# Performance work log

Hardware: AMD Instinct MI355X
Metric: run time of the kernel (lower is better)

Reference implementation:

```python
import jax, jax.numpy as jnp
import numpy as np
from jax import lax

NUM_MASKS = 100
NUM_CLASSES = 81  # 80 + 1
KERNEL_DIM = 256
BIAS_PRIOR = float(-np.log((1 - 0.01) / 0.01))


def setup_inputs() -> dict:
    key = jax.random.key(0)
    ks = jax.random.split(key, 12)
    B, C, H, W = 4, 256, 160, 160
    D = C  # expand_dim = in_channels * num_groups
    inp = {
        "features": jax.random.normal(ks[0], (B, C, H, W), jnp.float32),
        # iam_conv: Conv2d(C, num_masks, 3, padding=1)
        "w_iam": jax.random.normal(ks[1], (NUM_MASKS, C, 3, 3), jnp.float32) * 0.01,
        "b_iam": jnp.full((NUM_MASKS,), BIAS_PRIOR, jnp.float32),
        "softmax_bias": jnp.ones((1,), jnp.float32),
        # fc: Linear(D, D), xavier-ish
        "w_fc": jax.random.normal(ks[2], (D, D), jnp.float32) * (1.0 / np.sqrt(D)),
        "b_fc": jnp.zeros((D,), jnp.float32),
        "w_cls": jax.random.normal(ks[3], (NUM_CLASSES, D), jnp.float32) * 0.01,
        "b_cls": jnp.full((NUM_CLASSES,), BIAS_PRIOR, jnp.float32),
        "w_ker": jax.random.normal(ks[4], (KERNEL_DIM, D), jnp.float32) * 0.01,
        "b_ker": jnp.zeros((KERNEL_DIM,), jnp.float32),
        "w_obj": jax.random.normal(ks[5], (1, D), jnp.float32) * (1.0 / np.sqrt(D)),
        "b_obj": jnp.zeros((1,), jnp.float32),
        "w_box": jax.random.normal(ks[6], (4, D), jnp.float32) * 0.01,
        "b_box": jnp.zeros((4,), jnp.float32),
    }
    return inp


def reference(features, w_iam, b_iam, softmax_bias, w_fc, b_fc,
              w_cls, b_cls, w_ker, b_ker, w_obj, b_obj, w_box, b_box):
    B, C, H, W = features.shape
    # conv score map: (B, num_masks, H, W)
    iam = lax.conv_general_dilated(
        features, w_iam, window_strides=(1, 1), padding="SAME",
        dimension_numbers=("NCHW", "OIHW", "NCHW")) + b_iam[None, :, None, None]
    # num_groups == 1: single group iam
    iam_flat = iam.reshape(B, NUM_MASKS, H * W)
    # softmax over HW with learned scalar bias (bias shifts uniformly -> no-op math-wise but kept faithful)
    iam_prob = jax.nn.softmax(iam_flat + softmax_bias[0], axis=-1)  # (B, M, HW)
    # spatial attention pooling: bmm(prob, feats^T) -> (B, M, C)
    inst = jnp.einsum("bmp,bcp->bmc", iam_prob, features.reshape(B, C, H * W))
    # prev_inst_features is None -> skip fc_fuse
    inst = jax.nn.relu(inst @ w_fc.T + b_fc)
    pred_logits = inst @ w_cls.T + b_cls
    pred_kernel = inst @ w_ker.T + b_ker
    pred_scores = inst @ w_obj.T + b_obj
    pred_bboxes = inst @ w_box.T + b_box
    return (pred_logits, pred_kernel, pred_scores, pred_bboxes, iam, inst)
```

## Files before the change

### kernel.cpp

```cpp
#include <hip/hip_runtime.h>
#include <hip/hip_bf16.h>

typedef __attribute__((ext_vector_type(8))) short bf16x8;
typedef __attribute__((ext_vector_type(4))) float f32x4;

#define HW_ 25600
#define HP_ 162
#define WP_ 162

__device__ __forceinline__ unsigned short f2bf(float f) {
    union { float f; unsigned u; } x; x.f = f;
    unsigned r = x.u + 0x7FFFu + ((x.u >> 16) & 1u);
    return (unsigned short)(r >> 16);
}

typedef const __attribute__((address_space(1))) unsigned int* gas_t;
typedef __attribute__((address_space(3))) unsigned int* las_t;
__device__ __forceinline__ void gl_lds16(const void* g, void* l) {
    __builtin_amdgcn_global_load_lds((gas_t)g, (las_t)l, 16, 0, 0);
}

__global__ __launch_bounds__(256) void k_prep(const float* __restrict__ w_iam,
                                              unsigned short* __restrict__ wp,
                                              unsigned short* __restrict__ fpad) {
    int bid = blockIdx.x;
    if (bid < 1152) {
        int idx = bid * 256 + threadIdx.x;
        int stage = idx >> 12;
        int r = idx & 4095;
        int m = r >> 5, cl = r & 31;
        int tap = stage >> 3, kc = stage & 7;
        int jj = (cl >> 3) ^ ((m >> 1) & 3);
        int c = kc * 32 + jj * 8 + (cl & 7);
        int dy = (tap * 11) >> 5, dx = tap - dy * 3;
        float v = (m < 100) ? w_iam[((m * 256 + c) * 3 + dy) * 3 + dx] : 0.f;
        wp[idx] = f2bf(v);
    } else {
        int idx = (bid - 1152) * 256 + threadIdx.x;
        const int perb = 164864;
        if (idx >= 4 * perb) return;
        int b = idx / perb;
        int r = idx - b * perb;
        int hp, wpp, c;
        if (r < 82944) {
            hp = (r < 41472) ? 0 : 161;
            int r2 = r % 41472;
            wpp = r2 >> 8; c = r2 & 255;
        } else {
            r -= 82944;
            wpp = (r < 40960) ? 0 : 161;
            int r2 = r % 40960;
            hp = 1 + (r2 >> 8); c = r2 & 255;
        }
        fpad[((b * HP_ + hp) * WP_ + wpp) * 256 + c] = 0;
    }
}

__global__ __launch_bounds__(256) void k_convert(const float* __restrict__ feat,
                                                 unsigned short* __restrict__ fpad) {
    int bid = blockIdx.x;
    int b = bid / 640;
    int h = (bid >> 2) % 160;
    int c0 = (bid & 3) * 64;
    __shared__ float tile[64][161];
    int t = threadIdx.x;
    const float4* src4 = (const float4*)(feat + ((long)(b * 256 + c0) * 160 + h) * 160);
    #pragma unroll
    for (int s = 0; s < 10; ++s) {
        int q = t + s * 256;
        int ci = q / 40;
        int w4 = q - ci * 40;
        float4 v = src4[(long)ci * 6400 + w4];
        tile[ci][w4 * 4 + 0] = v.x;
        tile[ci][w4 * 4 + 1] = v.y;
        tile[ci][w4 * 4 + 2] = v.z;
        tile[ci][w4 * 4 + 3] = v.w;
    }
    __syncthreads();
    int co = (t & 7) * 8, wq = t >> 3;
    unsigned short* dst = fpad + ((long)(b * HP_ + h + 1) * WP_ + 1) * 256 + c0 + co;
    #pragma unroll
    for (int wp = 0; wp < 5; ++wp) {
        int w = wq + wp * 32;
        bf16x8 v;
        #pragma unroll
        for (int j = 0; j < 8; ++j) v[j] = (short)f2bf(tile[co + j][w]);
        *(bf16x8*)(dst + (long)w * 256) = v;
    }
}

__global__ __launch_bounds__(256, 3) void k_conv(const unsigned short* __restrict__ fpad,
                                                 const unsigned short* __restrict__ wprep,
                                                 const float* __restrict__ b_iam,
                                                 float* __restrict__ iam) {
    int bid = blockIdx.x;
    bid = (bid & 7) * 100 + (bid >> 3);
    int b = bid / 200;
    int p0 = (bid % 200) * 128;
    int tid = threadIdx.x;
    int lane = tid & 63, wid = tid >> 6;
    int wr = wid >> 1, wc = wid & 1;

    __shared__ __align__(16) unsigned short As[2][4096];
    __shared__ __align__(16) unsigned short Bs[2][4096];

    const unsigned short* fb = fpad + (long)b * HP_ * WP_ * 256;
    const unsigned short* gBsrc[2];
    {
        int swz = ((lane & 3) ^ ((lane >> 3) & 3)) * 8;
        #pragma unroll
        for (int i = 0; i < 2; ++i) {
            int pr = i * 64 + wid * 16 + (lane >> 2);
            int p = p0 + pr;
            int h = p / 160, w = p - h * 160;
            gBsrc[i] = fb + ((long)h * WP_ + w) * 256 + swz;
        }
    }
    const unsigned short* gA0 = wprep + (wid << 9) + (lane << 3);

    f32x4 acc[4][4];
    #pragma unroll
    for (int i = 0; i < 4; ++i)
        #pragma unroll
        for (int j = 0; j < 4; ++j)
            #pragma unroll
            for (int k = 0; k < 4; ++k) acc[i][j][k] = 0.f;

    int chB   = (((lane >> 4) ^ ((lane >> 1) & 3)) << 4);
    int aBase = (wr << 12) + ((lane & 15) << 6) + chB;
    int bBase = (wc << 12) + ((lane & 15) << 6) + chB;

    auto issue = [&](int s, int bi) {
        int tap = s >> 3, kc = s & 7;
        int dy = (tap * 11) >> 5, dx = tap - dy * 3;
        long boff = ((long)dy * WP_ + dx) * 256 + kc * 32;
        const unsigned short* ga = gA0 + ((long)s << 12);
        char* Ad = (char*)As[bi] + (wid << 10);
        char* Bd = (char*)Bs[bi] + (wid << 10);
        gl_lds16(ga, Ad);
        gl_lds16(ga + 2048, Ad + 4096);
        gl_lds16(gBsrc[0] + boff, Bd);
        gl_lds16(gBsrc[1] + boff, Bd + 4096);
    };

    auto compute = [&](int bi) {
        const char* Ab = (const char*)As[bi];
        const char* Bb = (const char*)Bs[bi];
        bf16x8 af[4], bfv[4];
        #pragma unroll
        for (int mf = 0; mf < 4; ++mf)
            af[mf] = *(const bf16x8*)(Ab + aBase + (mf << 10));
        #pragma unroll
        for (int nf = 0; nf < 4; ++nf)
            bfv[nf] = *(const bf16x8*)(Bb + bBase + (nf << 10));
        __builtin_amdgcn_s_setprio(1);
        #pragma unroll
        for (int mf = 0; mf < 4; ++mf)
            #pragma unroll
            for (int nf = 0; nf < 4; ++nf)
                acc[mf][nf] = __builtin_amdgcn_mfma_f32_16x16x32_bf16(
                    af[mf], bfv[nf], acc[mf][nf], 0, 0, 0);
        __builtin_amdgcn_s_setprio(0);
    };

    issue(0, 0);
    for (int s = 0; s < 71; ++s) {
        issue(s + 1, (s + 1) & 1);
        asm volatile("s_waitcnt vmcnt(4)" ::: "memory");
        __builtin_amdgcn_sched_barrier(0);
        __builtin_amdgcn_s_barrier();
        __builtin_amdgcn_sched_barrier(0);
        compute(s & 1);
        __builtin_amdgcn_sched_barrier(0);
        __builtin_amdgcn_s_barrier();
        __builtin_amdgcn_sched_barrier(0);
    }
    asm volatile("s_waitcnt vmcnt(0)" ::: "memory");
    __builtin_amdgcn_sched_barrier(0);
    __builtin_amdgcn_s_barrier();
    __builtin_amdgcn_sched_barrier(0);
    compute(1);

    float* dst = iam + (long)b * 100 * HW_;
    #pragma unroll
    for (int mf = 0; mf < 4; ++mf)
        #pragma unroll
        for (int nf = 0; nf < 4; ++nf) {
            int p = p0 + wc * 64 + nf * 16 + (lane & 15);
            int m0 = wr * 64 + mf * 16 + ((lane >> 4) << 2);
            #pragma unroll
            for (int j = 0; j < 4; ++j) {
                int m = m0 + j;
                if (m < 100) dst[(long)m * HW_ + p] = acc[mf][nf][j] + b_iam[m];
            }
        }
}

__global__ __launch_bounds__(256, 2) void k_pool(const float* __restrict__ feat,
                                                 const float* __restrict__ iam,
                                                 float* __restrict__ partials,
                                                 float* __restrict__ psum) {
    int bid = blockIdx.x;
    int b = bid / 100;
    int slice = bid - b * 100;
    int p0 = slice * 256;
    int tid = threadIdx.x, lane = tid & 63, wq = tid >> 6;

    __shared__ __align__(16) unsigned short A[128 * 72];
    __shared__ __align__(16) unsigned short Bl[256 * 72];
    __shared__ float sums[128];
    if (tid < 128) sums[tid] = 0.f;
    __syncthreads();

    f32x4 acc[7][4];
    #pragma unroll
    for (int i = 0; i < 7; ++i)
        #pragma unroll
        for (int j = 0; j < 4; ++j)
            #pragma unroll
            for (int k = 0; k < 4; ++k) acc[i][j][k] = 0.f;

    int kgrp = (lane >> 4) << 3;

    for (int ks = 0; ks < 4; ++ks) {
        int k0 = p0 + ks * 64;
        for (int s = 0; s < 4; ++s) {
            int q = tid + s * 256;
            int mi = q >> 3, j0 = (q & 7) * 8;
            bf16x8 o;
            if (mi < 100) {
                const float4* sp4 = (const float4*)(iam + (long)(b * 100 + mi) * HW_ + k0 + j0);
                float4 v0 = sp4[0], v1 = sp4[1];
                float xv[8] = {v0.x, v0.y, v0.z, v0.w, v1.x, v1.y, v1.z, v1.w};
                float ls = 0.f;
                #pragma unroll
                for (int j = 0; j < 8; ++j) {
                    float e = __expf(xv[j]);
                    o[j] = (short)f2bf(e);
                    ls += e;
                }
                atomicAdd(&sums[mi], ls);
            } else {
                #pragma unroll
                for (int j = 0; j < 8; ++j) o[j] = 0;
            }
            *(bf16x8*)(A + mi * 72 + j0) = o;
        }
        for (int s = 0; s < 8; ++s) {
            int q = tid + s * 256;
            int ci = q >> 3, j0 = (q & 7) * 8;
            const float4* sp4 = (const float4*)(feat + (long)(b * 256 + ci) * HW_ + k0 + j0);
            float4 v0 = sp4[0], v1 = sp4[1];
            float xv[8] = {v0.x, v0.y, v0.z, v0.w, v1.x, v1.y, v1.z, v1.w};
            bf16x8 o;
            #pragma unroll
            for (int j = 0; j < 8; ++j) o[j] = (short)f2bf(xv[j]);
            *(bf16x8*)(Bl + ci * 72 + j0) = o;
        }
        __syncthreads();
        #pragma unroll
        for (int kk = 0; kk < 64; kk += 32) {
            bf16x8 af[7], bfv[4];
            #pragma unroll
            for (int mf = 0; mf < 7; ++mf)
                af[mf] = *(const bf16x8*)(A + (mf * 16 + (lane & 15)) * 72 + kk + kgrp);
            #pragma unroll
            for (int nf = 0; nf < 4; ++nf)
                bfv[nf] = *(const bf16x8*)(Bl + (wq * 64 + nf * 16 + (lane & 15)) * 72 + kk + kgrp);
            #pragma unroll
            for (int mf = 0; mf < 7; ++mf)
                #pragma unroll
                for (int nf = 0; nf < 4; ++nf)
                    acc[mf][nf] = __builtin_amdgcn_mfma_f32_16x16x32_bf16(
                        af[mf], bfv[nf], acc[mf][nf], 0, 0, 0);
        }
        __syncthreads();
    }
    if (tid < 100) psum[(long)bid * 112 + tid] = sums[tid];
    float* dst = partials + (long)bid * 112 * 256;
    #pragma unroll
    for (int mf = 0; mf < 7; ++mf)
        #pragma unroll
        for (int nf = 0; nf < 4; ++nf) {
            int m0 = mf * 16 + ((lane >> 4) << 2);
            int c  = wq * 64 + nf * 16 + (lane & 15);
            #pragma unroll
            for (int j = 0; j < 4; ++j)
                dst[(long)(m0 + j) * 256 + c] = acc[mf][nf][j];
        }
}

__global__ __launch_bounds__(256) void k_redpool(const float* __restrict__ partials,
                                                 const float* __restrict__ psum,
                                                 float* __restrict__ inst_pool) {
    int bid = blockIdx.x;
    int b = bid / 100, m = bid - b * 100;
    int c = threadIdx.x;
    float s = 0.f, d = 0.f;
    for (int sl = 0; sl < 100; ++sl) {
        s += partials[((long)(b * 100 + sl) * 112 + m) * 256 + c];
        d += psum[(long)(b * 100 + sl) * 112 + m];
    }
    inst_pool[(long)bid * 256 + c] = s / d;
}

__global__ __launch_bounds__(256) void k_fc(const float* __restrict__ inst_pool,
                                            const float* __restrict__ w_fc, const float* __restrict__ b_fc,
                                            const float* __restrict__ w_cls, const float* __restrict__ b_cls,
                                            const float* __restrict__ w_ker, const float* __restrict__ b_ker,
                                            const float* __restrict__ w_obj, const float* __restrict__ b_obj,
                                            const float* __restrict__ w_box, const float* __restrict__ b_box,
                                            float* __restrict__ out) {
    int r = blockIdx.x;
    int t = threadIdx.x;
    __shared__ float row[256];
    __shared__ float inst_s[256];
    row[t] = inst_pool[(long)r * 256 + t];
    __syncthreads();
    {
        float acc = b_fc[t];
        const float4* wv = (const float4*)(w_fc + (long)t * 256);
        for (int c = 0; c < 64; ++c) {
            float4 w4 = wv[c];
            acc += w4.x * row[c * 4] + w4.y * row[c * 4 + 1] + w4.z * row[c * 4 + 2] + w4.w * row[c * 4 + 3];
        }
        acc = fmaxf(acc, 0.f);
        inst_s[t] = acc;
        out[10376800 + (long)r * 256 + t] = acc;
    }
    __syncthreads();
    {
        float acc = b_ker[t];
        const float4* wv = (const float4*)(w_ker + (long)t * 256);
        for (int c = 0; c < 64; ++c) {
            float4 w4 = wv[c];
            acc += w4.x * inst_s[c * 4] + w4.y * inst_s[c * 4 + 1] + w4.z * inst_s[c * 4 + 2] + w4.w * inst_s[c * 4 + 3];
        }
        out[32400 + (long)r * 256 + t] = acc;
    }
    if (t < 81) {
        float acc = b_cls[t];
        const float4* wv = (const float4*)(w_cls + (long)t * 256);
        for (int c = 0; c < 64; ++c) {
            float4 w4 = wv[c];
            acc += w4.x * inst_s[c * 4] + w4.y * inst_s[c * 4 + 1] + w4.z * inst_s[c * 4 + 2] + w4.w * inst_s[c * 4 + 3];
        }
        out[(long)r * 81 + t] = acc;
    }
    if (t == 0) {
        float acc = b_obj[0];
        for (int c = 0; c < 256; ++c) acc += w_obj[c] * inst_s[c];
        out[134800 + r] = acc;
    }
    if (t >= 1 && t < 5) {
        int j = t - 1;
        float acc = b_box[j];
        for (int c = 0; c < 256; ++c) acc += w_box[j * 256 + c] * inst_s[c];
        out[135200 + (long)r * 4 + j] = acc;
    }
}

extern "C" void kernel_launch(void* const* d_in, const int* in_sizes, int n_in,
                              void* d_out, int out_size, void* d_ws, size_t ws_size,
                              hipStream_t stream) {
    const float* feat  = (const float*)d_in[0];
    const float* w_iam = (const float*)d_in[1];
    const float* b_iam = (const float*)d_in[2];
    const float* w_fc  = (const float*)d_in[4];
    const float* b_fc  = (const float*)d_in[5];
    const float* w_cls = (const float*)d_in[6];
    const float* b_cls = (const float*)d_in[7];
    const float* w_ker = (const float*)d_in[8];
    const float* b_ker = (const float*)d_in[9];
    const float* w_obj = (const float*)d_in[10];
    const float* b_obj = (const float*)d_in[11];
    const float* w_box = (const float*)d_in[12];
    const float* b_box = (const float*)d_in[13];
    float* out = (float*)d_out;

    char* ws = (char*)d_ws;
    unsigned short* fpad  = (unsigned short*)ws;
    unsigned short* wprep = (unsigned short*)(ws + 53747712);
    float* partials  = (float*)ws;
    float* psum      = (float*)(ws + 45875200);
    float* inst_pool = (float*)(ws + 46054400);

    float* iam = out + 136800;

    k_prep   <<<dim3(3728), dim3(256), 0, stream>>>(w_iam, wprep, fpad);
    k_convert<<<dim3(2560), dim3(256), 0, stream>>>(feat, fpad);
    k_conv   <<<dim3(800),  dim3(256), 0, stream>>>(fpad, wprep, b_iam, iam);
    k_pool   <<<dim3(400),  dim3(256), 0, stream>>>(feat, iam, partials, psum);
    k_redpool<<<dim3(400),  dim3(256), 0, stream>>>(partials, psum, inst_pool);
    k_fc     <<<dim3(400),  dim3(256), 0, stream>>>(inst_pool, w_fc, b_fc, w_cls, b_cls,
                                                    w_ker, b_ker, w_obj, b_obj, w_box, b_box, out);
}
```

Measured before the change: 211.7 us.

## Reuse feature rows across horizontal conv taps and halve pool slices

The conv kernel now loads one feature row strip per (dy, kc) step, 130 padded pixels wide, and reads it at three horizontal offsets for the dx taps, along with the three dx weight slices. This cuts the main loop from 72 to 24 steps and removes the redundant B-tile loads of shifted pixels. Shared memory grows to about 66 KB, so occupancy is lowered to 2 blocks per SM. A row-wrap correction handles tiles that cross an image row. Separately, the pool kernel processes 512 pixels per block with 200 blocks, which halves the partials the reduce kernel must sum but leaves fewer blocks to fill the GPU.

```diff
diff --git a/kernel.cpp b/kernel.cpp
--- a/kernel.cpp
+++ b/kernel.cpp
@@ -89,7 +89,7 @@
     }
 }
 
-__global__ __launch_bounds__(256, 3) void k_conv(const unsigned short* __restrict__ fpad,
+__global__ __launch_bounds__(256, 2) void k_conv(const unsigned short* __restrict__ fpad,
                                                  const unsigned short* __restrict__ wprep,
                                                  const float* __restrict__ b_iam,
                                                  float* __restrict__ iam) {
@@ -101,22 +101,26 @@
     int lane = tid & 63, wid = tid >> 6;
     int wr = wid >> 1, wc = wid & 1;
 
-    __shared__ __align__(16) unsigned short As[2][4096];
-    __shared__ __align__(16) unsigned short Bs[2][4096];
-
+    __shared__ __align__(16) char smem[2][33024];
+
+    int h0 = p0 / 160, w0 = p0 - h0 * 160;
+    int istar = 160 - w0;
     const unsigned short* fb = fpad + (long)b * HP_ * WP_ * 256;
-    const unsigned short* gBsrc[2];
+
+    long rterm[2];
     {
-        int swz = ((lane & 3) ^ ((lane >> 3) & 3)) * 8;
+        int c = tid & 3;
         #pragma unroll
         for (int i = 0; i < 2; ++i) {
-            int pr = i * 64 + wid * 16 + (lane >> 2);
-            int p = p0 + pr;
-            int h = p / 160, w = p - h * 160;
-            gBsrc[i] = fb + ((long)h * WP_ + w) * 256 + swz;
-        }
-    }
-    const unsigned short* gA0 = wprep + (wid << 9) + (lane << 3);
+            int r = i * 64 + (tid >> 2);
+            rterm[i] = (long)r * 256 + ((c ^ ((r >> 1) & 3)) << 3);
+        }
+    }
+    long rterm2;
+    {
+        int r = 128 + ((lane & 15) >> 2), c = lane & 3;
+        rterm2 = (long)r * 256 + ((c ^ ((r >> 1) & 3)) << 3);
+    }
 
     f32x4 acc[4][4];
     #pragma unroll
@@ -126,47 +130,61 @@
             #pragma unroll
             for (int k = 0; k < 4; ++k) acc[i][j][k] = 0.f;
 
-    int chB   = (((lane >> 4) ^ ((lane >> 1) & 3)) << 4);
-    int aBase = (wr << 12) + ((lane & 15) << 6) + chB;
-    int bBase = (wc << 12) + ((lane & 15) << 6) + chB;
+    int aBase = (wr << 12) + ((lane & 15) << 6) + ((((lane >> 4) ^ ((lane >> 1) & 3))) << 4);
+    int rb[4];
+    #pragma unroll
+    for (int nf = 0; nf < 4; ++nf) {
+        int i = wc * 64 + nf * 16 + (lane & 15);
+        rb[nf] = i + 2 * (i >= istar);
+    }
 
     auto issue = [&](int s, int bi) {
-        int tap = s >> 3, kc = s & 7;
-        int dy = (tap * 11) >> 5, dx = tap - dy * 3;
-        long boff = ((long)dy * WP_ + dx) * 256 + kc * 32;
-        const unsigned short* ga = gA0 + ((long)s << 12);
-        char* Ad = (char*)As[bi] + (wid << 10);
-        char* Bd = (char*)Bs[bi] + (wid << 10);
-        gl_lds16(ga, Ad);
-        gl_lds16(ga + 2048, Ad + 4096);
-        gl_lds16(gBsrc[0] + boff, Bd);
-        gl_lds16(gBsrc[1] + boff, Bd + 4096);
+        int dy = s >> 3, kc = s & 7;
+        char* Ad = smem[bi];
+        char* Bd = smem[bi] + 24576;
+        #pragma unroll
+        for (int dx = 0; dx < 3; ++dx) {
+            const unsigned short* ga = wprep + ((long)((dy * 3 + dx) * 8 + kc) << 12) + (tid << 3);
+            char* Adst = Ad + (dx << 13) + (wid << 10);
+            gl_lds16(ga, Adst);
+            gl_lds16(ga + 2048, Adst + 4096);
+        }
+        long base = ((long)((h0 + dy) * WP_ + w0)) * 256 + (kc << 5);
+        gl_lds16(fb + base + rterm[0], Bd + (wid << 10));
+        gl_lds16(fb + base + rterm[1], Bd + 4096 + (wid << 10));
+        if (lane < 16) gl_lds16(fb + base + rterm2, Bd + 8192);
     };
 
     auto compute = [&](int bi) {
-        const char* Ab = (const char*)As[bi];
-        const char* Bb = (const char*)Bs[bi];
-        bf16x8 af[4], bfv[4];
-        #pragma unroll
-        for (int mf = 0; mf < 4; ++mf)
-            af[mf] = *(const bf16x8*)(Ab + aBase + (mf << 10));
-        #pragma unroll
-        for (int nf = 0; nf < 4; ++nf)
-            bfv[nf] = *(const bf16x8*)(Bb + bBase + (nf << 10));
-        __builtin_amdgcn_s_setprio(1);
-        #pragma unroll
-        for (int mf = 0; mf < 4; ++mf)
-            #pragma unroll
-            for (int nf = 0; nf < 4; ++nf)
-                acc[mf][nf] = __builtin_amdgcn_mfma_f32_16x16x32_bf16(
-                    af[mf], bfv[nf], acc[mf][nf], 0, 0, 0);
-        __builtin_amdgcn_s_setprio(0);
+        const char* Ab = smem[bi];
+        const char* Bb = smem[bi] + 24576;
+        #pragma unroll
+        for (int dx = 0; dx < 3; ++dx) {
+            bf16x8 af[4], bfv[4];
+            #pragma unroll
+            for (int mf = 0; mf < 4; ++mf)
+                af[mf] = *(const bf16x8*)(Ab + (dx << 13) + aBase + (mf << 10));
+            #pragma unroll
+            for (int nf = 0; nf < 4; ++nf) {
+                int row = rb[nf] + dx;
+                bfv[nf] = *(const bf16x8*)(Bb + (row << 6) +
+                            ((((lane >> 4) ^ ((row >> 1) & 3))) << 4));
+            }
+            __builtin_amdgcn_s_setprio(1);
+            #pragma unroll
+            for (int mf = 0; mf < 4; ++mf)
+                #pragma unroll
+                for (int nf = 0; nf < 4; ++nf)
+                    acc[mf][nf] = __builtin_amdgcn_mfma_f32_16x16x32_bf16(
+                        af[mf], bfv[nf], acc[mf][nf], 0, 0, 0);
+            __builtin_amdgcn_s_setprio(0);
+        }
     };
 
     issue(0, 0);
-    for (int s = 0; s < 71; ++s) {
+    for (int s = 0; s < 23; ++s) {
         issue(s + 1, (s + 1) & 1);
-        asm volatile("s_waitcnt vmcnt(4)" ::: "memory");
+        asm volatile("s_waitcnt vmcnt(9)" ::: "memory");
         __builtin_amdgcn_sched_barrier(0);
         __builtin_amdgcn_s_barrier();
         __builtin_amdgcn_sched_barrier(0);
@@ -201,9 +219,9 @@
                                                  float* __restrict__ partials,
                                                  float* __restrict__ psum) {
     int bid = blockIdx.x;
-    int b = bid / 100;
-    int slice = bid - b * 100;
-    int p0 = slice * 256;
+    int b = bid / 50;
+    int slice = bid - b * 50;
+    int p0 = slice * 512;
     int tid = threadIdx.x, lane = tid & 63, wq = tid >> 6;
 
     __shared__ __align__(16) unsigned short A[128 * 72];
@@ -222,7 +240,7 @@
 
     int kgrp = (lane >> 4) << 3;
 
-    for (int ks = 0; ks < 4; ++ks) {
+    for (int ks = 0; ks < 8; ++ks) {
         int k0 = p0 + ks * 64;
         for (int s = 0; s < 4; ++s) {
             int q = tid + s * 256;
@@ -297,9 +315,9 @@
     int b = bid / 100, m = bid - b * 100;
     int c = threadIdx.x;
     float s = 0.f, d = 0.f;
-    for (int sl = 0; sl < 100; ++sl) {
-        s += partials[((long)(b * 100 + sl) * 112 + m) * 256 + c];
-        d += psum[(long)(b * 100 + sl) * 112 + m];
+    for (int sl = 0; sl < 50; ++sl) {
+        s += partials[((long)(b * 50 + sl) * 112 + m) * 256 + c];
+        d += psum[(long)(b * 50 + sl) * 112 + m];
     }
     inst_pool[(long)bid * 256 + c] = s / d;
 }
@@ -382,15 +400,15 @@
     unsigned short* fpad  = (unsigned short*)ws;
     unsigned short* wprep = (unsigned short*)(ws + 53747712);
     float* partials  = (float*)ws;
-    float* psum      = (float*)(ws + 45875200);
-    float* inst_pool = (float*)(ws + 46054400);
+    float* psum      = (float*)(ws + 22937600);
+    float* inst_pool = (float*)(ws + 23027200);
 
     float* iam = out + 136800;
 
     k_prep   <<<dim3(3728), dim3(256), 0, stream>>>(w_iam, wprep, fpad);
     k_convert<<<dim3(2560), dim3(256), 0, stream>>>(feat, fpad);
     k_conv   <<<dim3(800),  dim3(256), 0, stream>>>(fpad, wprep, b_iam, iam);
-    k_pool   <<<dim3(400),  dim3(256), 0, stream>>>(feat, iam, partials, psum);
+    k_pool   <<<dim3(200),  dim3(256), 0, stream>>>(feat, iam, partials, psum);
     k_redpool<<<dim3(400),  dim3(256), 0, stream>>>(partials, psum, inst_pool);
     k_fc     <<<dim3(400),  dim3(256), 0, stream>>>(inst_pool, w_fc, b_fc, w_cls, b_cls,
                                                     w_ker, b_ker, w_obj, b_obj, w_box, b_box, out);
```

Result: faster. 191.6 us (-9.5%).
